# Kernel tuning notes

Measured on AMD Instinct MI355X. Metric: run time of the kernel, lower is better.

## Reference

```python
import jax, jax.numpy as jnp
import numpy as np

EMA_ALPHA = 0.1


def setup_inputs() -> dict:
    key = jax.random.key(0)
    k1, k2, k3 = jax.random.split(key, 3)
    B, N, D = 4, 128, 4096
    T, K = 32768, 8
    memory = jax.random.normal(k1, (B, N, D), dtype=jnp.float32)
    hidden_states = jax.random.normal(k2, (T, D), dtype=jnp.float32)
    slot_indices = jax.random.randint(k3, (T, K), 0, N, dtype=jnp.int64)
    return {
        "memory": memory,
        "hidden_states": hidden_states,
        "slot_indices": slot_indices,
        "batch_idx": 1,
    }


def reference(memory, hidden_states, slot_indices, batch_idx):
    # memory: [B, N, D]; hidden_states: [T, D]; slot_indices: [T, K] int
    N = memory.shape[1]
    # Token t touches slot n if ANY of its top-K indices equals n
    # (mirrors torch (slot_indices == idx).any(dim=-1); duplicates in K count once)
    touch = (slot_indices[..., None] == jnp.arange(N)).any(axis=1)  # [T, N] bool
    m = touch.astype(hidden_states.dtype)                           # [T, N]
    counts = m.sum(axis=0)                                          # [N]
    sums = jnp.einsum("tn,td->nd", m, hidden_states)                # [N, D]
    agg = sums / jnp.maximum(counts, 1.0)[:, None]                  # masked mean per slot
    cur = memory[batch_idx]                                         # [N, D]
    upd = EMA_ALPHA * agg + (1.0 - EMA_ALPHA) * cur
    new_row = jnp.where((counts > 0)[:, None], upd, cur)            # untouched slots unchanged
    return memory.at[batch_idx].set(new_row)
```

## Files before the change

### kernel.cpp

```cpp
#include <hip/hip_runtime.h>
#include <hip/hip_bf16.h>

#define T_TOK   32768
#define N_SLOTS 128
#define D_DIM   4096
#define B_DIM   4

#define NCHUNK  16
#define CTOK    (T_TOK / NCHUNK)
#define KB      64
#define NT      (CTOK / KB)
#define WCOLS   256
#define NSLICE  (D_DIM / WCOLS)
#define THREADS 512

typedef unsigned long long u64;
typedef __attribute__((ext_vector_type(8))) short short8;
typedef __attribute__((ext_vector_type(4))) float f32x4;

#define PARTIAL_BYTES ((size_t)NCHUNK * N_SLOTS * D_DIM * 4)
#define COUNTS_OFF    PARTIAL_BYTES

#define BAR_LGKM() do { \
    asm volatile("s_waitcnt lgkmcnt(0)" ::: "memory"); \
    __builtin_amdgcn_s_barrier(); \
  } while (0)

__device__ __forceinline__ unsigned int pack_bf2(float lo, float hi) {
  unsigned short a = __bfloat16_as_ushort(__float2bfloat16(lo));
  unsigned short b = __bfloat16_as_ushort(__float2bfloat16(hi));
  return (unsigned int)a | ((unsigned int)b << 16);
}

__global__ __launch_bounds__(256) void prep_kernel(const int* __restrict__ sidx,
                                                   int* __restrict__ counts) {
  __shared__ int cnt[N_SLOTS];
  const int tid = threadIdx.x;
  if (tid < N_SLOTS) cnt[tid] = 0;
  __syncthreads();

  const int t = blockIdx.x * 256 + tid;
  const int4 a = ((const int4*)sidx)[2 * t];
  const int4 b = ((const int4*)sidx)[2 * t + 1];
  int idx[8] = {a.x, a.y, a.z, a.w, b.x, b.y, b.z, b.w};

  #pragma unroll
  for (int k = 0; k < 8; ++k) {
    int n = idx[k];
    bool dup = false;
    #pragma unroll
    for (int j = 0; j < 8; ++j)
      if (j < k) dup |= (idx[j] == n);
    if (!dup && (unsigned)n < (unsigned)N_SLOTS) atomicAdd(&cnt[n], 1);
  }
  __syncthreads();
  if (tid < N_SLOTS && cnt[tid] > 0) atomicAdd(&counts[tid], cnt[tid]);
}

__global__ __launch_bounds__(THREADS, 2) void sums_kernel(
    const float* __restrict__ hidden, const int* __restrict__ sidx,
    float* __restrict__ partial) {
  __shared__ unsigned int   h_w[2][WCOLS * 32];
  __shared__ unsigned short m_u[2][N_SLOTS * KB];

  const int tid = threadIdx.x;
  const int slice = blockIdx.x & (NSLICE - 1);
  const int chunk = blockIdx.x / NSLICE;
  const int d0 = slice * WCOLS;
  const int cb = chunk * CTOK;

  const int kp = tid & 31;
  const int cg = tid >> 5;

  const int tok0 = tid >> 3;

  const int lane = tid & 63;
  const int wv   = tid >> 6;
  const int l15  = lane & 15;
  const int lk   = lane >> 4;

  f32x4 acc[8][2];
  #pragma unroll
  for (int i = 0; i < 8; ++i)
    #pragma unroll
    for (int j = 0; j < 2; ++j)
      acc[i][j] = (f32x4){0.f, 0.f, 0.f, 0.f};

  float4 fa[4], fb[4];
  int s0;

  {
    const float* hp = hidden + (size_t)(cb + 2 * kp) * D_DIM + d0 + cg * 16;
    #pragma unroll
    for (int q = 0; q < 4; ++q) {
      fa[q] = ((const float4*)hp)[q];
      fb[q] = ((const float4*)(hp + D_DIM))[q];
    }
    s0 = sidx[cb * 8 + tid];
  }

  for (int t = 0; t < NT; ++t) {
    const int b = t & 1;
    const int cs0 = s0;

    #pragma unroll
    for (int q = 0; q < 4; ++q) {
      const int colbase = cg * 16 + q * 4;
      const float ax[4] = {fa[q].x, fa[q].y, fa[q].z, fa[q].w};
      const float bx[4] = {fb[q].x, fb[q].y, fb[q].z, fb[q].w};
      #pragma unroll
      for (int c = 0; c < 4; ++c) {
        const int col = colbase + c;
        h_w[b][col * 32 + (kp ^ ((col & 7) << 2))] = pack_bf2(ax[c], bx[c]);
      }
    }

    if (t + 1 < NT) {
      const int tb = cb + (t + 1) * KB;
      const float* hp = hidden + (size_t)(tb + 2 * kp) * D_DIM + d0 + cg * 16;
      #pragma unroll
      for (int q = 0; q < 4; ++q) {
        fa[q] = ((const float4*)hp)[q];
        fb[q] = ((const float4*)(hp + D_DIM))[q];
      }
      s0 = sidx[tb * 8 + tid];
    }

    {
      uint4* mz = (uint4*)m_u[b];
      const uint4 z = make_uint4(0, 0, 0, 0);
      mz[tid] = z;
      mz[THREADS + tid] = z;
    }
    BAR_LGKM();

    {
      const int n0 = cs0 & (N_SLOTS - 1);
      m_u[b][n0 * 64 + (tok0 ^ ((n0 & 7) << 3))] = 0x3F80;
    }
    BAR_LGKM();

    {
      const unsigned short* mb = m_u[b];
      const unsigned short* hb = (const unsigned short*)h_w[b];
      #pragma unroll
      for (int ks = 0; ks < 2; ++ks) {
        const int kbase = ks * 32 + lk * 8;
        const int col0 = (wv * 2) * 16 + l15;
        const int col1 = (wv * 2 + 1) * 16 + l15;
        const short8 bf0 = *(const short8*)&hb[col0 * 64 + (kbase ^ ((col0 & 7) << 3))];
        const short8 bf1 = *(const short8*)&hb[col1 * 64 + (kbase ^ ((col1 & 7) << 3))];
        #pragma unroll
        for (int mt = 0; mt < 8; ++mt) {
          const int row = mt * 16 + l15;
          const short8 af = *(const short8*)&mb[row * 64 + (kbase ^ ((row & 7) << 3))];
          acc[mt][0] = __builtin_amdgcn_mfma_f32_16x16x32_bf16(af, bf0, acc[mt][0], 0, 0, 0);
          acc[mt][1] = __builtin_amdgcn_mfma_f32_16x16x32_bf16(af, bf1, acc[mt][1], 0, 0, 0);
        }
      }
    }
  }

  float* pbase = partial + (size_t)chunk * N_SLOTS * D_DIM;
  #pragma unroll
  for (int mt = 0; mt < 8; ++mt)
    #pragma unroll
    for (int j = 0; j < 2; ++j) {
      const int col = d0 + (wv * 2 + j) * 16 + l15;
      #pragma unroll
      for (int r = 0; r < 4; ++r) {
        const int row = mt * 16 + lk * 4 + r;
        pbase[(size_t)row * D_DIM + col] = acc[mt][j][r];
      }
    }
}

__global__ __launch_bounds__(256) void final_kernel(const float* __restrict__ memory,
                                                    const float* __restrict__ partial,
                                                    const int* __restrict__ counts,
                                                    const int* __restrict__ bidx_p,
                                                    float* __restrict__ out) {
  const size_t i = (size_t)blockIdx.x * 256 + threadIdx.x;
  float4 v = ((const float4*)memory)[i];
  const size_t rowLen4 = (size_t)N_SLOTS * (D_DIM / 4);
  const size_t rowStart = (size_t)(*bidx_p) * rowLen4;
  if (i >= rowStart && i < rowStart + rowLen4) {
    const size_t rel = i - rowStart;
    const int n  = (int)(rel / (D_DIM / 4));
    const int d4 = (int)(rel % (D_DIM / 4));
    const int c = counts[n];
    if (c > 0) {
      const float4* p4 = (const float4*)partial;
      float4 s = {0.f, 0.f, 0.f, 0.f};
      #pragma unroll
      for (int ch = 0; ch < NCHUNK; ++ch) {
        float4 p = p4[((size_t)ch * N_SLOTS + n) * (D_DIM / 4) + d4];
        s.x += p.x; s.y += p.y; s.z += p.z; s.w += p.w;
      }
      const float w = 0.1f / (float)c;
      v.x = s.x * w + 0.9f * v.x;
      v.y = s.y * w + 0.9f * v.y;
      v.z = s.z * w + 0.9f * v.z;
      v.w = s.w * w + 0.9f * v.w;
    }
  }
  ((float4*)out)[i] = v;
}

extern "C" void kernel_launch(void* const* d_in, const int* in_sizes, int n_in,
                              void* d_out, int out_size, void* d_ws, size_t ws_size,
                              hipStream_t stream) {
  const float* memory = (const float*)d_in[0];
  const float* hidden = (const float*)d_in[1];
  const int*   sidx   = (const int*)d_in[2];
  const int*   bidx   = (const int*)d_in[3];
  float* out = (float*)d_out;

  char* ws = (char*)d_ws;
  float* partial = (float*)ws;
  int*   counts  = (int*)(ws + COUNTS_OFF);

  hipMemsetAsync(counts, 0, 512, stream);

  prep_kernel<<<T_TOK / 256, 256, 0, stream>>>(sidx, counts);

  sums_kernel<<<NCHUNK * NSLICE, THREADS, 0, stream>>>(hidden, sidx, partial);

  const int totalVec4 = B_DIM * N_SLOTS * (D_DIM / 4);
  final_kernel<<<totalVec4 / 256, 256, 0, stream>>>(memory, partial, counts, bidx, out);
}
```

Measured before the change: 124.2 us.

## Widen sums tiles to 1024 threads, single m buffer, bf16 partials

Doubles the column slice per block and the number of token chunks, and runs 1024-thread blocks with a single-buffered slot mask guarded by an extra barrier. Partial sums are stored as bf16 rather than fp32 to halve per-chunk bytes, and the final kernel reduces 32 chunks. The intent is better reuse of the mask fragment across more columns and less partial traffic per chunk. In exchange LDS use grows, occupancy drops, more synchronisation is added and precision is lost in the partials.

```diff
diff --git a/kernel.cpp b/kernel.cpp
--- a/kernel.cpp
+++ b/kernel.cpp
@@ -6,19 +6,19 @@
 #define D_DIM   4096
 #define B_DIM   4
 
-#define NCHUNK  16
+#define NCHUNK  32
 #define CTOK    (T_TOK / NCHUNK)
 #define KB      64
 #define NT      (CTOK / KB)
-#define WCOLS   256
+#define WCOLS   512
 #define NSLICE  (D_DIM / WCOLS)
-#define THREADS 512
+#define THREADS 1024
 
 typedef unsigned long long u64;
 typedef __attribute__((ext_vector_type(8))) short short8;
 typedef __attribute__((ext_vector_type(4))) float f32x4;
 
-#define PARTIAL_BYTES ((size_t)NCHUNK * N_SLOTS * D_DIM * 4)
+#define PARTIAL_BYTES ((size_t)NCHUNK * N_SLOTS * D_DIM * 2)
 #define COUNTS_OFF    PARTIAL_BYTES
 
 #define BAR_LGKM() do { \
@@ -30,6 +30,9 @@
   unsigned short a = __bfloat16_as_ushort(__float2bfloat16(lo));
   unsigned short b = __bfloat16_as_ushort(__float2bfloat16(hi));
   return (unsigned int)a | ((unsigned int)b << 16);
+}
+__device__ __forceinline__ unsigned short bf16u(float x) {
+  return __bfloat16_as_ushort(__float2bfloat16(x));
 }
 
 __global__ __launch_bounds__(256) void prep_kernel(const int* __restrict__ sidx,
@@ -57,11 +60,11 @@
   if (tid < N_SLOTS && cnt[tid] > 0) atomicAdd(&counts[tid], cnt[tid]);
 }
 
-__global__ __launch_bounds__(THREADS, 2) void sums_kernel(
+__global__ __launch_bounds__(THREADS) void sums_kernel(
     const float* __restrict__ hidden, const int* __restrict__ sidx,
-    float* __restrict__ partial) {
+    unsigned short* __restrict__ partial) {
   __shared__ unsigned int   h_w[2][WCOLS * 32];
-  __shared__ unsigned short m_u[2][N_SLOTS * KB];
+  __shared__ unsigned short m_u[N_SLOTS * KB];
 
   const int tid = threadIdx.x;
   const int slice = blockIdx.x & (NSLICE - 1);
@@ -87,7 +90,7 @@
       acc[i][j] = (f32x4){0.f, 0.f, 0.f, 0.f};
 
   float4 fa[4], fb[4];
-  int s0;
+  int s0 = 0;
 
   {
     const float* hp = hidden + (size_t)(cb + 2 * kp) * D_DIM + d0 + cg * 16;
@@ -96,7 +99,7 @@
       fa[q] = ((const float4*)hp)[q];
       fb[q] = ((const float4*)(hp + D_DIM))[q];
     }
-    s0 = sidx[cb * 8 + tid];
+    if (tid < 512) s0 = sidx[cb * 8 + tid];
   }
 
   for (int t = 0; t < NT; ++t) {
@@ -123,25 +126,22 @@
         fa[q] = ((const float4*)hp)[q];
         fb[q] = ((const float4*)(hp + D_DIM))[q];
       }
-      s0 = sidx[tb * 8 + tid];
-    }
+      if (tid < 512) s0 = sidx[tb * 8 + tid];
+    }
+
+    BAR_LGKM();
+
+    ((uint4*)m_u)[tid] = make_uint4(0, 0, 0, 0);
+    BAR_LGKM();
+
+    if (tid < 512) {
+      const int n0 = cs0 & (N_SLOTS - 1);
+      m_u[n0 * 64 + (tok0 ^ ((n0 & 7) << 3))] = 0x3F80;
+    }
+    BAR_LGKM();
 
     {
-      uint4* mz = (uint4*)m_u[b];
-      const uint4 z = make_uint4(0, 0, 0, 0);
-      mz[tid] = z;
-      mz[THREADS + tid] = z;
-    }
-    BAR_LGKM();
-
-    {
-      const int n0 = cs0 & (N_SLOTS - 1);
-      m_u[b][n0 * 64 + (tok0 ^ ((n0 & 7) << 3))] = 0x3F80;
-    }
-    BAR_LGKM();
-
-    {
-      const unsigned short* mb = m_u[b];
+      const unsigned short* mb = m_u;
       const unsigned short* hb = (const unsigned short*)h_w[b];
       #pragma unroll
       for (int ks = 0; ks < 2; ++ks) {
@@ -161,7 +161,7 @@
     }
   }
 
-  float* pbase = partial + (size_t)chunk * N_SLOTS * D_DIM;
+  unsigned short* pbase = partial + (size_t)chunk * N_SLOTS * D_DIM;
   #pragma unroll
   for (int mt = 0; mt < 8; ++mt)
     #pragma unroll
@@ -170,13 +170,13 @@
       #pragma unroll
       for (int r = 0; r < 4; ++r) {
         const int row = mt * 16 + lk * 4 + r;
-        pbase[(size_t)row * D_DIM + col] = acc[mt][j][r];
+        pbase[(size_t)row * D_DIM + col] = bf16u(acc[mt][j][r]);
       }
     }
 }
 
 __global__ __launch_bounds__(256) void final_kernel(const float* __restrict__ memory,
-                                                    const float* __restrict__ partial,
+                                                    const unsigned short* __restrict__ partial,
                                                     const int* __restrict__ counts,
                                                     const int* __restrict__ bidx_p,
                                                     float* __restrict__ out) {
@@ -190,12 +190,14 @@
     const int d4 = (int)(rel % (D_DIM / 4));
     const int c = counts[n];
     if (c > 0) {
-      const float4* p4 = (const float4*)partial;
       float4 s = {0.f, 0.f, 0.f, 0.f};
       #pragma unroll
       for (int ch = 0; ch < NCHUNK; ++ch) {
-        float4 p = p4[((size_t)ch * N_SLOTS + n) * (D_DIM / 4) + d4];
-        s.x += p.x; s.y += p.y; s.z += p.z; s.w += p.w;
+        const ushort4 p = ((const ushort4*)partial)[((size_t)ch * N_SLOTS + n) * (D_DIM / 4) + d4];
+        s.x += __uint_as_float((unsigned int)p.x << 16);
+        s.y += __uint_as_float((unsigned int)p.y << 16);
+        s.z += __uint_as_float((unsigned int)p.z << 16);
+        s.w += __uint_as_float((unsigned int)p.w << 16);
       }
       const float w = 0.1f / (float)c;
       v.x = s.x * w + 0.9f * v.x;
@@ -217,8 +219,8 @@
   float* out = (float*)d_out;
 
   char* ws = (char*)d_ws;
-  float* partial = (float*)ws;
-  int*   counts  = (int*)(ws + COUNTS_OFF);
+  unsigned short* partial = (unsigned short*)ws;
+  int* counts = (int*)(ws + COUNTS_OFF);
 
   hipMemsetAsync(counts, 0, 512, stream);
 
```

Result: slower. 164.3 us (+32.2%).
